# Kernel tuning notes

Hardware: AMD Instinct MI355X
Metric: run time of the kernel (lower is better)

The kernel has to match this reference:

```python
import jax, jax.numpy as jnp
import numpy as np

B, C, H, W = 4, 2048, 48, 48
HC = 256

def setup_inputs() -> dict:
    key = jax.random.key(0)
    k1, k2, k3, k4 = jax.random.split(key, 4)
    scale = 1.0 / np.sqrt(C)
    return {
        "left_features": jax.random.normal(k1, (B, C, H, W), dtype=jnp.float32),
        "right_features": jax.random.normal(k2, (B, C, H, W), dtype=jnp.float32),
        "Wq": jax.random.normal(k3, (HC, C), dtype=jnp.float32) * scale,
        "bq": jnp.zeros((HC,), dtype=jnp.float32),
        "Wk": jax.random.normal(k4, (HC, C), dtype=jnp.float32) * scale,
        "bk": jnp.zeros((HC,), dtype=jnp.float32),
    }

def _coattn(query_feat, ref_feat, Wq, bq, Wk, bk):
    b, c, h, w = query_feat.shape
    hw = h * w
    # 1x1 convs == per-pixel channel projections
    Q = jnp.einsum('bchw,oc->bohw', query_feat, Wq) + bq[None, :, None, None]
    K = jnp.einsum('bchw,oc->bohw', ref_feat, Wk) + bk[None, :, None, None]
    Qf = Q.reshape(b, -1, hw)          # [b, hc, hw_q]
    Kf = K.reshape(b, -1, hw)          # [b, hc, hw_k]
    V = ref_feat.reshape(b, c, hw)     # [b, c, hw_k]
    # attention scores over all spatial pairs, softmax over reference positions
    attn = jax.nn.softmax(jnp.einsum('bci,bcj->bij', Qf, Kf), axis=-1)  # [b, hw_q, hw_k]
    out = jnp.einsum('bij,bcj->bci', attn, V)  # [b, c, hw_q]
    return out.reshape(b, c, h, w)

def reference(left_features, right_features, Wq, bq, Wk, bk):
    weighted_r = _coattn(left_features, right_features, Wq, bq, Wk, bk)
    weighted_l = _coattn(right_features, left_features, Wq, bq, Wk, bk)
    # rearrange '[orig, weighted] two b c h w -> b (two c) h w' == channel concat
    left_attended = jnp.concatenate([left_features, weighted_l], axis=1)
    right_attended = jnp.concatenate([right_features, weighted_r], axis=1)
    return (left_attended, right_attended)
```

## Files before the change

kernel.cpp:

```cpp
#include <hip/hip_runtime.h>
#include <stdint.h>


#define NB 4
#define NC 2048
#define NHW 2304
#define NHC 256
#define NT 36

typedef _Float16 f16;
typedef __attribute__((ext_vector_type(4))) _Float16 f16x4;
typedef __attribute__((ext_vector_type(8))) _Float16 f16x8;
typedef __attribute__((ext_vector_type(4))) float f32x4;

static __device__ __forceinline__ void glds16(const void* g, void* lds) {
  __builtin_amdgcn_global_load_lds(
      (const __attribute__((address_space(1))) uint32_t*)g,
      (__attribute__((address_space(3))) uint32_t*)lds, 16, 0, 0);
}

__global__ __launch_bounds__(256) void k_prep(
    const float* __restrict__ xl, const float* __restrict__ xr,
    float* __restrict__ out, f16* __restrict__ Xh, f16* __restrict__ Xt) {
  const int z = blockIdx.z, side = z >> 2, b = z & 3;
  const float* X = (side ? xr : xl) + (size_t)b * NC * NHW;
  const int hw0 = blockIdx.x * 64, c0 = blockIdx.y * 64;
  const int t = threadIdx.x;
  const int colb = (t & 15) * 4;
  const int r0 = t >> 4;
  __shared__ f16 Lt[64 * 64];
  float* outb = out + (size_t)side * ((size_t)NB * 2 * NC * NHW) + (size_t)b * (2 * NC * NHW);
  f16* Xhb = Xh + (size_t)side * ((size_t)NB * NC * NHW) + (size_t)b * NC * NHW;
  f16* Xtb = Xt + (size_t)side * ((size_t)NB * NHW * NC) + (size_t)b * NHW * NC;
#pragma unroll
  for (int p = 0; p < 4; ++p) {
    int r = r0 + p * 16;
    size_t go = (size_t)(c0 + r) * NHW + hw0 + colb;
    float4 v = *(const float4*)&X[go];
    *(float4*)&outb[go] = v;
    f16x4 h; h[0] = (f16)v.x; h[1] = (f16)v.y; h[2] = (f16)v.z; h[3] = (f16)v.w;
    *(f16x4*)&Xhb[go] = h;
#pragma unroll
    for (int j = 0; j < 4; ++j) {
      int row = colb + j;
      int byte = row * 128 + ((r * 2) ^ ((((row >> 2) & 7)) << 4));
      *(f16*)((char*)Lt + byte) = h[j];
    }
  }
  __syncthreads();
#pragma unroll
  for (int p = 0; p < 2; ++p) {
    int idx = p * 256 + t;
    int row = idx >> 3, ch = idx & 7;
    int byte = row * 128 + (((ch ^ ((row >> 2) & 7))) << 4);
    f16x8 vv = *(const f16x8*)((char*)Lt + byte);
    *(f16x8*)&Xtb[(size_t)(hw0 + row) * NC + c0 + ch * 8] = vv;
  }
}

__global__ __launch_bounds__(256) void k_w16(
    const float* __restrict__ wq, const float* __restrict__ wk, f16* __restrict__ Ws) {
  const int N4 = NHC * NC / 4;
  int idx = blockIdx.x * 256 + threadIdx.x;
  const float* src = (idx < N4) ? wq : wk;
  int e4 = (idx < N4) ? idx : idx - N4;
  float4 v = ((const float4*)src)[e4];
  f16x4 h; h[0] = (f16)v.x; h[1] = (f16)v.y; h[2] = (f16)v.z; h[3] = (f16)v.w;
  ((f16x4*)Ws)[idx] = h;
}

__global__ __launch_bounds__(256) void k_proj(
    const f16* __restrict__ Ws, const f16* __restrict__ Xt0,
    const float* __restrict__ bq, const float* __restrict__ bk,
    f16* __restrict__ Yt0) {
  __shared__ f16 LA[2][128 * 32], LB[2][128 * 32];
  const int side = blockIdx.z;
  const f16* Xt = Xt0 + (size_t)side * ((size_t)NB * NHW * NC);
  f16* Yt = Yt0 + (size_t)side * ((size_t)NB * NHW * 512);
  const int n0 = blockIdx.x * 128;
  const int m0 = blockIdx.y * 128;
  const int tid = threadIdx.x, wv = tid >> 6, ln = tid & 63;
  const int lr = ln & 15, lh = ln >> 4;
  const int wm = wv >> 1, wn = wv & 1;
  f32x4 acc[4][4];
#pragma unroll
  for (int mi = 0; mi < 4; ++mi)
#pragma unroll
    for (int ni = 0; ni < 4; ++ni)
#pragma unroll
      for (int q = 0; q < 4; ++q) acc[mi][ni][q] = 0.f;

  auto stage = [&](int bi, int ks) {
    int k0 = ks * 32;
#pragma unroll
    for (int rep = 0; rep < 2; ++rep) {
      int u = rep * 256 + wv * 64 + ln;
      int r = u >> 2, k8 = (u & 3) * 8;
      int ub8 = (rep * 256 + wv * 64) * 8;
      glds16(Ws + (size_t)(m0 + r) * NC + k0 + k8, &LA[bi][ub8]);
      glds16(Xt + (size_t)(n0 + r) * NC + k0 + k8, &LB[bi][ub8]);
    }
  };
  auto compute = [&](int bi) {
    f16x8 af[4], bf[4];
#pragma unroll
    for (int mi = 0; mi < 4; ++mi)
      af[mi] = *(const f16x8*)&LA[bi][(wm * 64 + mi * 16 + lr) * 32 + lh * 8];
#pragma unroll
    for (int ni = 0; ni < 4; ++ni)
      bf[ni] = *(const f16x8*)&LB[bi][(wn * 64 + ni * 16 + lr) * 32 + lh * 8];
#pragma unroll
    for (int mi = 0; mi < 4; ++mi)
#pragma unroll
      for (int ni = 0; ni < 4; ++ni)
        acc[mi][ni] = __builtin_amdgcn_mfma_f32_16x16x32_f16(af[mi], bf[ni], acc[mi][ni], 0, 0, 0);
  };

  stage(0, 0);
  __syncthreads();
  int cur = 0;
  for (int ks = 0; ks < 63; ++ks) {
    stage(cur ^ 1, ks + 1);
    compute(cur);
    __syncthreads();
    cur ^= 1;
  }
  compute(cur);

#pragma unroll
  for (int mi = 0; mi < 4; ++mi)
#pragma unroll
    for (int ni = 0; ni < 4; ++ni) {
      int ob = m0 + wm * 64 + mi * 16 + lh * 4;
      int i = n0 + wn * 64 + ni * 16 + lr;
      f16x4 hv;
#pragma unroll
      for (int q = 0; q < 4; ++q) {
        int o = ob + q;
        float bias = (o < NHC) ? bq[o] : bk[o - NHC];
        hv[q] = (f16)(acc[mi][ni][q] + bias);
      }
      *(f16x4*)&Yt[(size_t)i * 512 + ob] = hv;
    }
}

__global__ __launch_bounds__(256) void k_scores(
    const f16* __restrict__ Yt, float* __restrict__ S0, float* __restrict__ S1,
    int dir0) {
  __shared__ f16 LA[2][128 * 32], LB[2][128 * 32];
  const size_t YTS = (size_t)NB * NHW * 512;
  const int z = blockIdx.z;
  const int dir = dir0 + (z >> 2);
  const int b = z & 3;
  const int i0 = blockIdx.x * 128, j0 = blockIdx.y * 128;
  const int tid = threadIdx.x, wv = tid >> 6, ln = tid & 63;
  const int lr = ln & 15, lh = ln >> 4;
  const int wm = wv >> 1, wn = wv & 1;
  const f16* Qb = Yt + (size_t)dir * YTS + (size_t)b * NHW * 512;
  const f16* Kb = Yt + (size_t)(1 - dir) * YTS + NHC + (size_t)b * NHW * 512;
  f32x4 acc[4][4];
#pragma unroll
  for (int mi = 0; mi < 4; ++mi)
#pragma unroll
    for (int ni = 0; ni < 4; ++ni)
#pragma unroll
      for (int q = 0; q < 4; ++q) acc[mi][ni][q] = 0.f;

  auto stage = [&](int bi, int ks) {
    int k0 = ks * 32;
#pragma unroll
    for (int rep = 0; rep < 2; ++rep) {
      int u = rep * 256 + wv * 64 + ln;
      int r = u >> 2, k8 = (u & 3) * 8;
      int ub8 = (rep * 256 + wv * 64) * 8;
      glds16(Qb + (size_t)(i0 + r) * 512 + k0 + k8, &LA[bi][ub8]);
      glds16(Kb + (size_t)(j0 + r) * 512 + k0 + k8, &LB[bi][ub8]);
    }
  };
  auto compute = [&](int bi) {
    f16x8 af[4], bf[4];
#pragma unroll
    for (int mi = 0; mi < 4; ++mi)
      af[mi] = *(const f16x8*)&LA[bi][(wm * 64 + mi * 16 + lr) * 32 + lh * 8];
#pragma unroll
    for (int ni = 0; ni < 4; ++ni)
      bf[ni] = *(const f16x8*)&LB[bi][(wn * 64 + ni * 16 + lr) * 32 + lh * 8];
#pragma unroll
    for (int mi = 0; mi < 4; ++mi)
#pragma unroll
      for (int ni = 0; ni < 4; ++ni)
        acc[mi][ni] = __builtin_amdgcn_mfma_f32_16x16x32_f16(af[mi], bf[ni], acc[mi][ni], 0, 0, 0);
  };

  stage(0, 0);
  __syncthreads();
  int cur = 0;
  for (int ks = 0; ks < 7; ++ks) {
    stage(cur ^ 1, ks + 1);
    compute(cur);
    __syncthreads();
    cur ^= 1;
  }
  compute(cur);

  float* Sb = (dir ? S1 : S0) + (size_t)b * NHW * NHW;
#pragma unroll
  for (int mi = 0; mi < 4; ++mi)
#pragma unroll
    for (int ni = 0; ni < 4; ++ni) {
      int i = i0 + wm * 64 + mi * 16 + lh * 4;
      int j = j0 + wn * 64 + ni * 16 + lr;
#pragma unroll
      for (int q = 0; q < 4; ++q)
        Sb[(size_t)(i + q) * NHW + j] = acc[mi][ni][q];
    }
}

__global__ __launch_bounds__(256) void k_softmax(
    float* __restrict__ S0, float* __restrict__ S1) {
  const int rid = blockIdx.x;
  const int ROWS = NB * NHW;
  float* rp = (rid < ROWS ? S0 : S1) + (size_t)(rid < ROWS ? rid : rid - ROWS) * NHW;
  const int t = threadIdx.x;
  float v[9];
  float m = -3.4e38f;
#pragma unroll
  for (int k = 0; k < 9; ++k) { v[k] = rp[t + 256 * k]; m = fmaxf(m, v[k]); }
#pragma unroll
  for (int off = 32; off > 0; off >>= 1) m = fmaxf(m, __shfl_xor(m, off));
  __shared__ float red[4];
  __shared__ float red2[4];
  const int wv = t >> 6, ln = t & 63;
  if (ln == 0) red[wv] = m;
  __syncthreads();
  m = fmaxf(fmaxf(red[0], red[1]), fmaxf(red[2], red[3]));
  float s = 0.f;
#pragma unroll
  for (int k = 0; k < 9; ++k) { v[k] = expf(v[k] - m); s += v[k]; }
#pragma unroll
  for (int off = 32; off > 0; off >>= 1) s += __shfl_xor(s, off);
  if (ln == 0) red2[wv] = s;
  __syncthreads();
  float inv = 1.0f / (red2[0] + red2[1] + red2[2] + red2[3]);
  f16* op = (f16*)rp;
#pragma unroll
  for (int k = 0; k < 9; ++k) op[t + 256 * k] = (f16)(v[k] * inv);
}

__global__ __launch_bounds__(512, 2) void k_pv8(
    const f16* __restrict__ V0, const f16* __restrict__ V1,
    const float* __restrict__ S0, const float* __restrict__ S1,
    float* __restrict__ out, int ndirs, long long ob0, long long ob1) {
  extern __shared__ __align__(16) f16 SH[];

  const int nwg = ndirs * 384;
  const int bid = blockIdx.x;
  const int wg = (bid & 7) * (nwg >> 3) + (bid >> 3);
  const int n = wg % 12;
  const int r1 = wg / 12;
  const int m = r1 & 7;
  const int r2 = r1 >> 3;
  const int b = r2 & 3;
  const int dir = r2 >> 2;

  const f16* Vb = (dir ? V1 : V0) + (size_t)b * NC * NHW;
  const char* Sb = (const char*)(dir ? S1 : S0) + (size_t)b * NHW * NHW * 4;
  const long long obase = dir ? ob1 : ob0;
  const int c0 = m * 256, i0 = n * 192;
  const int tid = threadIdx.x, wv = tid >> 6, ln = tid & 63;
  const int lr = ln & 15, lg = ln >> 4;
  const int wm = wv >> 2, wn = wv & 3;

  const int fr = tid >> 3;
  const int scolb = ((tid & 7) * 16) ^ ((fr & 7) << 4);
  const f16* aSrc = Vb + (size_t)(c0 + fr) * NHW + (scolb >> 1);
  const char* bSrc = Sb + (size_t)(i0 + fr) * 9216 + scolb;
  const int ldsW = wv * 512;

  auto stA = [&](int bf, int t2, int r) {
    glds16(aSrc + (size_t)r * 64 * NHW + (size_t)t2 * 64,
           SH + bf * 16384 + r * 4096 + ldsW);
  };
  auto stB = [&](int bf, int t2, int r) {
    glds16(bSrc + (size_t)r * 64 * 9216 + t2 * 128,
           SH + 32768 + bf * 12288 + r * 4096 + ldsW);
  };
  auto rdA = [&](int bf, int mi, int ks) -> f16x8 {
    int row = wm * 128 + mi * 16 + lr;
    int colb = (ks * 64 + lg * 16) ^ ((row & 7) << 4);
    return *(const f16x8*)((const char*)(SH + bf * 16384) + row * 128 + colb);
  };
  auto rdB = [&](int bf, int ni, int ks) -> f16x8 {
    int row = wn * 48 + ni * 16 + lr;
    int colb = (ks * 64 + lg * 16) ^ ((row & 7) << 4);
    return *(const f16x8*)((const char*)(SH + 32768 + bf * 12288) + row * 128 + colb);
  };

  f32x4 acc[8][3];
#pragma unroll
  for (int mi = 0; mi < 8; ++mi)
#pragma unroll
    for (int ni = 0; ni < 3; ++ni)
#pragma unroll
      for (int q = 0; q < 4; ++q) acc[mi][ni][q] = 0.f;

  f16x8 Af[4][2], Bn0[2][2], Bn1[1][2];

#pragma unroll
  for (int r = 0; r < 4; ++r) stA(0, 0, r);
#pragma unroll
  for (int r = 0; r < 3; ++r) stB(0, 0, r);
#pragma unroll
  for (int r = 0; r < 4; ++r) stA(1, 1, r);
#pragma unroll
  for (int r = 0; r < 3; ++r) stB(1, 1, r);
  asm volatile("s_waitcnt vmcnt(7)" ::: "memory");
  asm volatile("s_barrier" ::: "memory");

  for (int t = 0; t < NT; ++t) {
    const int cb = t & 1;
    const bool s2 = (t + 2 < NT);
#pragma unroll
    for (int mi = 0; mi < 4; ++mi) { Af[mi][0] = rdA(cb, mi, 0); Af[mi][1] = rdA(cb, mi, 1); }
#pragma unroll
    for (int ni = 0; ni < 2; ++ni) { Bn0[ni][0] = rdB(cb, ni, 0); Bn0[ni][1] = rdB(cb, ni, 1); }
    asm volatile("s_barrier" ::: "memory");
    asm volatile("s_waitcnt lgkmcnt(0)" ::: "memory");
    __builtin_amdgcn_sched_barrier(0);
    __builtin_amdgcn_s_setprio(1);
#pragma unroll
    for (int ks = 0; ks < 2; ++ks)
#pragma unroll
      for (int mi = 0; mi < 4; ++mi)
#pragma unroll
        for (int ni = 0; ni < 2; ++ni)
          acc[mi][ni] = __builtin_amdgcn_mfma_f32_16x16x32_f16(Af[mi][ks], Bn0[ni][ks], acc[mi][ni], 0, 0, 0);
    __builtin_amdgcn_s_setprio(0);
    asm volatile("s_barrier" ::: "memory");
    Bn1[0][0] = rdB(cb, 2, 0); Bn1[0][1] = rdB(cb, 2, 1);
    if (s2) { stA(cb, t + 2, 0); stA(cb, t + 2, 2); }
    asm volatile("s_barrier" ::: "memory");
    asm volatile("s_waitcnt lgkmcnt(0)" ::: "memory");
    __builtin_amdgcn_sched_barrier(0);
    __builtin_amdgcn_s_setprio(1);
#pragma unroll
    for (int ks = 0; ks < 2; ++ks)
#pragma unroll
      for (int mi = 0; mi < 4; ++mi)
        acc[mi][2] = __builtin_amdgcn_mfma_f32_16x16x32_f16(Af[mi][ks], Bn1[0][ks], acc[mi][2], 0, 0, 0);
    __builtin_amdgcn_s_setprio(0);
    asm volatile("s_barrier" ::: "memory");
#pragma unroll
    for (int mi = 0; mi < 4; ++mi) { Af[mi][0] = rdA(cb, 4 + mi, 0); Af[mi][1] = rdA(cb, 4 + mi, 1); }
    if (s2) { stB(cb, t + 2, 0); stB(cb, t + 2, 1); }
    asm volatile("s_barrier" ::: "memory");
    asm volatile("s_waitcnt lgkmcnt(0)" ::: "memory");
    __builtin_amdgcn_sched_barrier(0);
    __builtin_amdgcn_s_setprio(1);
#pragma unroll
    for (int ks = 0; ks < 2; ++ks)
#pragma unroll
      for (int mi = 0; mi < 4; ++mi)
        acc[4 + mi][2] = __builtin_amdgcn_mfma_f32_16x16x32_f16(Af[mi][ks], Bn1[0][ks], acc[4 + mi][2], 0, 0, 0);
    __builtin_amdgcn_s_setprio(0);
    asm volatile("s_barrier" ::: "memory");
    if (s2) { stA(cb, t + 2, 1); stA(cb, t + 2, 3); stB(cb, t + 2, 2); }
    __builtin_amdgcn_s_setprio(1);
#pragma unroll
    for (int ks = 0; ks < 2; ++ks)
#pragma unroll
      for (int mi = 0; mi < 4; ++mi)
#pragma unroll
        for (int ni = 0; ni < 2; ++ni)
          acc[4 + mi][ni] = __builtin_amdgcn_mfma_f32_16x16x32_f16(Af[mi][ks], Bn0[ni][ks], acc[4 + mi][ni], 0, 0, 0);
    __builtin_amdgcn_s_setprio(0);
    if (s2)                { asm volatile("s_waitcnt vmcnt(7)" ::: "memory"); }
    else if (t + 1 < NT)   { asm volatile("s_waitcnt vmcnt(0)" ::: "memory"); }
    asm volatile("s_barrier" ::: "memory");
  }

  float* ob = out + obase + (size_t)b * (2 * NC * NHW);
#pragma unroll
  for (int mi = 0; mi < 8; ++mi)
#pragma unroll
    for (int ni = 0; ni < 3; ++ni) {
      int c = c0 + wm * 128 + mi * 16 + lg * 4;
      int i = i0 + wn * 48 + ni * 16 + lr;
#pragma unroll
      for (int q = 0; q < 4; ++q)
        ob[(size_t)(NC + c + q) * NHW + i] = acc[mi][ni][q];
    }
}

extern "C" void kernel_launch(void* const* d_in, const int* in_sizes, int n_in,
                              void* d_out, int out_size, void* d_ws, size_t ws_size,
                              hipStream_t stream) {
  const float* xl = (const float*)d_in[0];
  const float* xr = (const float*)d_in[1];
  const float* wq = (const float*)d_in[2];
  const float* bq = (const float*)d_in[3];
  const float* wk = (const float*)d_in[4];
  const float* bk = (const float*)d_in[5];
  float* out = (float*)d_out;
  char* ws = (char*)d_ws;

  const size_t XH_BYTES = (size_t)2 * NB * NC * NHW * 2;
  const size_t WS_BYTES = (size_t)512 * NC * 2;
  const size_t YT_BYTES = (size_t)2 * NB * NHW * 512 * 2;
  const size_t S_BYTES  = (size_t)NB * NHW * NHW * 4;

  f16* Xh = (f16*)ws;
  f16* Ws_ = (f16*)(ws + XH_BYTES);
  f16* Yt = (f16*)(ws + XH_BYTES + WS_BYTES);
  char* rest = ws + XH_BYTES + WS_BYTES + YT_BYTES;

  const size_t xh_side = (size_t)NB * NC * NHW;
  const long long obA = (long long)NB * 2 * NC * NHW;
  const long long obB = 0;

  const bool merged = ws_size >= XH_BYTES + WS_BYTES + YT_BYTES + 2 * S_BYTES;

  if (merged) {
    float* S0 = (float*)rest;
    char* rest2 = rest + S_BYTES;
    f16* Xt = (f16*)rest2;
    float* S1 = (float*)rest2;

    k_prep<<<dim3(36, 32, 8), dim3(256), 0, stream>>>(xl, xr, out, Xh, Xt);
    k_w16<<<dim3(1024), dim3(256), 0, stream>>>(wq, wk, Ws_);
    k_proj<<<dim3(72, 4, 2), dim3(256), 0, stream>>>(Ws_, Xt, bq, bk, Yt);

    k_scores<<<dim3(18, 18, 8), dim3(256), 0, stream>>>(Yt, S0, S1, 0);
    k_softmax<<<dim3(2 * NB * NHW), dim3(256), 0, stream>>>(S0, S1);
    k_pv8<<<dim3(768), dim3(512), 114688, stream>>>(
        Xh + xh_side, Xh, S0, S1, out, 2, obA, obB);
  } else {
    f16* Xt = (f16*)rest;
    float* S = (float*)rest;

    k_prep<<<dim3(36, 32, 8), dim3(256), 0, stream>>>(xl, xr, out, Xh, Xt);
    k_w16<<<dim3(1024), dim3(256), 0, stream>>>(wq, wk, Ws_);
    k_proj<<<dim3(72, 4, 2), dim3(256), 0, stream>>>(Ws_, Xt, bq, bk, Yt);

    k_scores<<<dim3(18, 18, 4), dim3(256), 0, stream>>>(Yt, S, S, 0);
    k_softmax<<<dim3(NB * NHW), dim3(256), 0, stream>>>(S, S);
    k_pv8<<<dim3(384), dim3(512), 114688, stream>>>(
        Xh + xh_side, Xh + xh_side, S, S, out, 1, obA, obA);

    k_scores<<<dim3(18, 18, 4), dim3(256), 0, stream>>>(Yt, S, S, 1);
    k_softmax<<<dim3(NB * NHW), dim3(256), 0, stream>>>(S, S);
    k_pv8<<<dim3(384), dim3(512), 114688, stream>>>(
        Xh, Xh, S, S, out, 1, obB, obB);
  }
}
```

Baseline: 423.2 us.

## Restructure GEMM main loop into two MFMA phases with split prefetch schedule

Reorganizes the inner loop of the attention-output GEMM from four MFMA phases with five barriers into two phases (top and bottom halves of the M tile), each using all three B fragments. Half of the A tile for step t+1 is now issued at the start of the iteration, and the rest of A plus all of B for step t+2 is issued after the first phase, with the vmcnt wait thresholds adjusted to match. The aim is fewer barriers and larger MFMA bursts per synchronization point. The cost is more live registers (two A fragment sets plus three B fragments) and a different global-to-LDS overlap pattern whose buffer-reuse correctness depends on the new barrier placement.

```diff
diff --git a/kernel.cpp b/kernel.cpp
--- a/kernel.cpp
+++ b/kernel.cpp
@@ -304,26 +304,25 @@
 #pragma unroll
       for (int q = 0; q < 4; ++q) acc[mi][ni][q] = 0.f;
 
-  f16x8 Af[4][2], Bn0[2][2], Bn1[1][2];
+  f16x8 A0f[4][2], A1f[4][2], Bf[3][2];
 
 #pragma unroll
   for (int r = 0; r < 4; ++r) stA(0, 0, r);
 #pragma unroll
   for (int r = 0; r < 3; ++r) stB(0, 0, r);
-#pragma unroll
-  for (int r = 0; r < 4; ++r) stA(1, 1, r);
+  stA(1, 1, 0); stA(1, 1, 2);
 #pragma unroll
   for (int r = 0; r < 3; ++r) stB(1, 1, r);
-  asm volatile("s_waitcnt vmcnt(7)" ::: "memory");
+  asm volatile("s_waitcnt vmcnt(5)" ::: "memory");
   asm volatile("s_barrier" ::: "memory");
 
   for (int t = 0; t < NT; ++t) {
-    const int cb = t & 1;
-    const bool s2 = (t + 2 < NT);
-#pragma unroll
-    for (int mi = 0; mi < 4; ++mi) { Af[mi][0] = rdA(cb, mi, 0); Af[mi][1] = rdA(cb, mi, 1); }
-#pragma unroll
-    for (int ni = 0; ni < 2; ++ni) { Bn0[ni][0] = rdB(cb, ni, 0); Bn0[ni][1] = rdB(cb, ni, 1); }
+    const int cb = t & 1, nb = cb ^ 1;
+#pragma unroll
+    for (int mi = 0; mi < 4; ++mi) { A0f[mi][0] = rdA(cb, mi, 0); A0f[mi][1] = rdA(cb, mi, 1); }
+#pragma unroll
+    for (int ni = 0; ni < 3; ++ni) { Bf[ni][0] = rdB(cb, ni, 0); Bf[ni][1] = rdB(cb, ni, 1); }
+    if (t + 1 < NT) { stA(nb, t + 1, 1); stA(nb, t + 1, 3); }
     asm volatile("s_barrier" ::: "memory");
     asm volatile("s_waitcnt lgkmcnt(0)" ::: "memory");
     __builtin_amdgcn_sched_barrier(0);
@@ -333,12 +332,16 @@
 #pragma unroll
       for (int mi = 0; mi < 4; ++mi)
 #pragma unroll
-        for (int ni = 0; ni < 2; ++ni)
-          acc[mi][ni] = __builtin_amdgcn_mfma_f32_16x16x32_f16(Af[mi][ks], Bn0[ni][ks], acc[mi][ni], 0, 0, 0);
+        for (int ni = 0; ni < 3; ++ni)
+          acc[mi][ni] = __builtin_amdgcn_mfma_f32_16x16x32_f16(A0f[mi][ks], Bf[ni][ks], acc[mi][ni], 0, 0, 0);
     __builtin_amdgcn_s_setprio(0);
     asm volatile("s_barrier" ::: "memory");
-    Bn1[0][0] = rdB(cb, 2, 0); Bn1[0][1] = rdB(cb, 2, 1);
-    if (s2) { stA(cb, t + 2, 0); stA(cb, t + 2, 2); }
+#pragma unroll
+    for (int mi = 0; mi < 4; ++mi) { A1f[mi][0] = rdA(cb, 4 + mi, 0); A1f[mi][1] = rdA(cb, 4 + mi, 1); }
+    if (t + 2 < NT) {
+      stA(cb, t + 2, 0); stA(cb, t + 2, 2);
+      stB(cb, t + 2, 0); stB(cb, t + 2, 1); stB(cb, t + 2, 2);
+    }
     asm volatile("s_barrier" ::: "memory");
     asm volatile("s_waitcnt lgkmcnt(0)" ::: "memory");
     __builtin_amdgcn_sched_barrier(0);
@@ -347,35 +350,12 @@
     for (int ks = 0; ks < 2; ++ks)
 #pragma unroll
       for (int mi = 0; mi < 4; ++mi)
-        acc[mi][2] = __builtin_amdgcn_mfma_f32_16x16x32_f16(Af[mi][ks], Bn1[0][ks], acc[mi][2], 0, 0, 0);
+#pragma unroll
+        for (int ni = 0; ni < 3; ++ni)
+          acc[4 + mi][ni] = __builtin_amdgcn_mfma_f32_16x16x32_f16(A1f[mi][ks], Bf[ni][ks], acc[4 + mi][ni], 0, 0, 0);
     __builtin_amdgcn_s_setprio(0);
-    asm volatile("s_barrier" ::: "memory");
-#pragma unroll
-    for (int mi = 0; mi < 4; ++mi) { Af[mi][0] = rdA(cb, 4 + mi, 0); Af[mi][1] = rdA(cb, 4 + mi, 1); }
-    if (s2) { stB(cb, t + 2, 0); stB(cb, t + 2, 1); }
-    asm volatile("s_barrier" ::: "memory");
-    asm volatile("s_waitcnt lgkmcnt(0)" ::: "memory");
-    __builtin_amdgcn_sched_barrier(0);
-    __builtin_amdgcn_s_setprio(1);
-#pragma unroll
-    for (int ks = 0; ks < 2; ++ks)
-#pragma unroll
-      for (int mi = 0; mi < 4; ++mi)
-        acc[4 + mi][2] = __builtin_amdgcn_mfma_f32_16x16x32_f16(Af[mi][ks], Bn1[0][ks], acc[4 + mi][2], 0, 0, 0);
-    __builtin_amdgcn_s_setprio(0);
-    asm volatile("s_barrier" ::: "memory");
-    if (s2) { stA(cb, t + 2, 1); stA(cb, t + 2, 3); stB(cb, t + 2, 2); }
-    __builtin_amdgcn_s_setprio(1);
-#pragma unroll
-    for (int ks = 0; ks < 2; ++ks)
-#pragma unroll
-      for (int mi = 0; mi < 4; ++mi)
-#pragma unroll
-        for (int ni = 0; ni < 2; ++ni)
-          acc[4 + mi][ni] = __builtin_amdgcn_mfma_f32_16x16x32_f16(Af[mi][ks], Bn0[ni][ks], acc[4 + mi][ni], 0, 0, 0);
-    __builtin_amdgcn_s_setprio(0);
-    if (s2)                { asm volatile("s_waitcnt vmcnt(7)" ::: "memory"); }
-    else if (t + 1 < NT)   { asm volatile("s_waitcnt vmcnt(0)" ::: "memory"); }
+    if (t + 2 < NT)      { asm volatile("s_waitcnt vmcnt(5)" ::: "memory"); }
+    else if (t + 1 < NT) { asm volatile("s_waitcnt vmcnt(0)" ::: "memory"); }
     asm volatile("s_barrier" ::: "memory");
   }
 
```

Measured after the change: 423.4 us. Within noise of the previous version (+0.0%).
